# Optimization experiments

Hardware: AMD Instinct MI355X
Metric: run time of the kernel (lower is better)

## Reference

```python
import jax, jax.numpy as jnp
import numpy as np

SEQ, HID = 4096, 1024
NEG_INF = -10000000000.0


def setup_inputs() -> dict:
    key = jax.random.key(0)
    ks = jax.random.split(key, 6)
    s = 1.0 / np.sqrt(HID)
    return {
        "query": jax.random.normal(ks[0], (SEQ, HID), jnp.float32),
        "key": jax.random.normal(ks[1], (SEQ, HID), jnp.float32),
        "value": jax.random.normal(ks[2], (SEQ, HID), jnp.float32),
        # SASRec causal mask: allowed positions are 1, masked are 0
        "mask": jnp.tril(jnp.ones((SEQ, SEQ), jnp.int32)),
        "Wq": jax.random.normal(ks[3], (HID, HID), jnp.float32) * s,
        "Wk": jax.random.normal(ks[4], (HID, HID), jnp.float32) * s,
        "Wv": jax.random.normal(ks[5], (HID, HID), jnp.float32) * s,
    }


def reference(query, key, value, mask, Wq, Wk, Wv):
    # nn.Linear(bias=False): y = x @ W.T
    Q = query @ Wq.T   # [S, H]
    K = key @ Wk.T     # [S, H]
    V = value @ Wv.T   # [S, H]
    scale = jnp.sqrt(jnp.asarray(HID, Q.dtype))
    energy = (Q @ K.T) / scale                      # [S, S]
    energy = jnp.where(mask == 0, NEG_INF, energy)  # masked_fill
    attention = jax.nn.softmax(energy, axis=-1)     # [S, S]
    x = attention @ V                               # dropout is identity in eval
    return (x, attention)
```

## Files before the change

### kernel.cpp

```cpp
#include <hip/hip_runtime.h>

#define SEQ 4096
#define HID 1024

typedef _Float16 f16x4 __attribute__((ext_vector_type(4)));
typedef _Float16 f16x8 __attribute__((ext_vector_type(8)));
typedef float    f32x4 __attribute__((ext_vector_type(4)));

__device__ __forceinline__ void gld16(const void* g, void* l) {
    __builtin_amdgcn_global_load_lds(
        (const __attribute__((address_space(1))) unsigned int*)g,
        (__attribute__((address_space(3))) unsigned int*)l, 16, 0, 0);
}

__global__ __launch_bounds__(256) void cast_all(
    const float4* __restrict__ q, const float4* __restrict__ k,
    const float4* __restrict__ v,
    const float4* __restrict__ wq, const float4* __restrict__ wk,
    const float4* __restrict__ wv,
    f16x4* __restrict__ qh, f16x4* __restrict__ kh, f16x4* __restrict__ vh,
    f16x4* __restrict__ wqh, f16x4* __restrict__ wkh, f16x4* __restrict__ wvh,
    float4* __restrict__ zx,
    int nX4, int nW4, int nZ4) {
    int t = blockIdx.x * 256 + threadIdx.x;
    const float4 *a, *b, *c; f16x4 *da, *db, *dc; int idx;
    if (t < nX4) { a = q; b = k; c = v; da = qh; db = kh; dc = vh; idx = t; }
    else if (t < nX4 + nW4) {
        idx = t - nX4;
        a = wq; b = wk; c = wv; da = wqh; db = wkh; dc = wvh;
    } else {
        idx = t - nX4 - nW4;
        if (idx < nZ4) zx[idx] = float4{0.f, 0.f, 0.f, 0.f};
        return;
    }
    float4 va = a[idx], vb = b[idx], vc = c[idx];
    f16x4 oa = {(_Float16)va.x, (_Float16)va.y, (_Float16)va.z, (_Float16)va.w};
    f16x4 ob = {(_Float16)vb.x, (_Float16)vb.y, (_Float16)vb.z, (_Float16)vb.w};
    f16x4 oc = {(_Float16)vc.x, (_Float16)vc.y, (_Float16)vc.z, (_Float16)vc.w};
    da[idx] = oa; db[idx] = ob; dc[idx] = oc;
}

__global__ __launch_bounds__(256) void transpose_f16(
    const _Float16* __restrict__ src, _Float16* __restrict__ dst,
    int R, int C) {
    __shared__ _Float16 tile[32][33];
    int c0 = blockIdx.x * 32, r0 = blockIdx.y * 32;
    int tr = threadIdx.x >> 5, tc = threadIdx.x & 31;
#pragma unroll
    for (int q = 0; q < 4; ++q)
        tile[tr + q * 8][tc] = src[(size_t)(r0 + tr + q * 8) * C + c0 + tc];
    __syncthreads();
#pragma unroll
    for (int q = 0; q < 4; ++q)
        dst[(size_t)(c0 + tr + q * 8) * R + r0 + tc] = tile[tc][tr + q * 8];
}

template <typename OutT, bool TRI_SKIP, bool TRI_K, int ZMODE>
__global__ __launch_bounds__(256) void gemm_nt(
    const _Float16* __restrict__ A, const _Float16* __restrict__ Bt,
    OutT* __restrict__ C, int M, int N, int K, float scale,
    long sA, long sB, long sC, int KC) {
    __shared__ __attribute__((aligned(16))) _Float16 As[2 * 128 * 32];
    __shared__ __attribute__((aligned(16))) _Float16 Bs[2 * 128 * 32];

    int bm = blockIdx.y;
    const int bn = blockIdx.x;
    if (TRI_SKIP && bn > bm) return;
    if (ZMODE == 1) {
        A  += (long)blockIdx.z * sA;
        Bt += (long)blockIdx.z * sB;
        C  += (long)blockIdx.z * sC;
    }

    int kstart = 0, kend;
    bool single = false;
    if (ZMODE == 3) {
        int y = 143 - (int)blockIdx.y;
        int g = 0;
        while (2 * (g + 1) * (g + 2) <= y) ++g;
        const int rem = y - 2 * g * (g + 1);
        const int m   = g + 1;
        const int rg  = rem / m;
        bm = 4 * g + rg;
        const int zc = rem - rg * m;
        kstart = zc * KC;
        kend   = min((bm + 1) * 128, kstart + KC);
        single = (m == 1);
    } else {
        kend = TRI_K ? min(K, (bm + 1) * 128) : K;
        if (ZMODE == 2) {
            kstart = blockIdx.z * KC;
            if (kstart >= kend) return;
            single = (kend <= KC);
            kend = min(kend, kstart + KC);
        }
    }

    const int tid = threadIdx.x;
    const int tr  = tid >> 2;
    const int tc8 = (tid & 3) * 8;

    const _Float16* Ab = A  + (size_t)bm * 128 * K;
    const _Float16* Bb = Bt + (size_t)bn * 128 * K;

    const int wave = tid >> 6;
    const int lane = tid & 63;
    const int wm = (wave >> 1) * 64;
    const int wn = (wave & 1) * 64;
    const int lr = lane & 15;
    const int lk = (lane >> 4) * 8;

    f32x4 acc[4][4];
#pragma unroll
    for (int i = 0; i < 4; ++i)
#pragma unroll
        for (int j = 0; j < 4; ++j) acc[i][j] = (f32x4)0.0f;

    for (int k0 = kstart; k0 < kend; k0 += 64) {
#pragma unroll
        for (int h = 0; h < 2; ++h) {
            const int kk = k0 + h * 32, off = h * 4096;
            gld16(Ab + (size_t)tr * K        + kk + tc8, &As[off + tr * 32 + tc8]);
            gld16(Ab + (size_t)(64 + tr) * K + kk + tc8, &As[off + (64 + tr) * 32 + tc8]);
            gld16(Bb + (size_t)tr * K        + kk + tc8, &Bs[off + tr * 32 + tc8]);
            gld16(Bb + (size_t)(64 + tr) * K + kk + tc8, &Bs[off + (64 + tr) * 32 + tc8]);
        }
        __syncthreads();

#pragma unroll
        for (int h = 0; h < 2; ++h) {
            const int off = h * 4096;
            f16x8 af[4], bfr[4];
#pragma unroll
            for (int i = 0; i < 4; ++i)
                af[i] = *(const f16x8*)&As[off + (wm + i * 16 + lr) * 32 + lk];
#pragma unroll
            for (int j = 0; j < 4; ++j)
                bfr[j] = *(const f16x8*)&Bs[off + (wn + j * 16 + lr) * 32 + lk];
#pragma unroll
            for (int i = 0; i < 4; ++i)
#pragma unroll
                for (int j = 0; j < 4; ++j)
                    acc[i][j] = __builtin_amdgcn_mfma_f32_16x16x32_f16(
                        af[i], bfr[j], acc[i][j], 0, 0, 0);
        }
        __syncthreads();
    }

    const int er = (lane >> 4) * 4;
    const int ec = lane & 15;
#pragma unroll
    for (int i = 0; i < 4; ++i) {
#pragma unroll
        for (int j = 0; j < 4; ++j) {
            const int row0 = bm * 128 + wm + i * 16 + er;
            const int col  = bn * 128 + wn + j * 16 + ec;
#pragma unroll
            for (int r = 0; r < 4; ++r) {
                const size_t idx = (size_t)(row0 + r) * N + col;
                const float val = acc[i][j][r] * scale;
                if (ZMODE >= 2 && !single)
                    atomicAdd((float*)&C[idx], val);
                else
                    C[idx] = (OutT)val;
            }
        }
    }
}

__global__ __launch_bounds__(256) void softmax_causal(
    _Float16* __restrict__ EP, float* __restrict__ att, int S) {
    __shared__ float rowbuf[SEQ];
    __shared__ float red[8];
    const int i   = blockIdx.x;
    const int tid = threadIdx.x;
    const int wv  = tid >> 6, ln = tid & 63;
    _Float16* Erow = EP + (size_t)i * S;

    float lmax = -INFINITY;
    for (int j8 = tid * 8; j8 <= i; j8 += 2048) {
        f16x8 e8 = *(const f16x8*)&Erow[j8];
#pragma unroll
        for (int u = 0; u < 8; ++u) {
            int j = j8 + u;
            if (j <= i) {
                float vv = (float)e8[u];
                rowbuf[j] = vv;
                lmax = fmaxf(lmax, vv);
            }
        }
    }
#pragma unroll
    for (int o = 32; o > 0; o >>= 1) lmax = fmaxf(lmax, __shfl_down(lmax, o, 64));
    if (ln == 0) red[wv] = lmax;
    __syncthreads();
    if (tid == 0)
        red[4] = fmaxf(fmaxf(red[0], red[1]), fmaxf(red[2], red[3]));
    __syncthreads();
    const float rmax = red[4];

    float lsum = 0.0f;
    for (int j4 = tid * 4; j4 <= i; j4 += 1024) {
        float4 e = *(float4*)&rowbuf[j4];
        float4 o;
        o.x = (j4     <= i) ? __expf(e.x - rmax) : 0.f;
        o.y = (j4 + 1 <= i) ? __expf(e.y - rmax) : 0.f;
        o.z = (j4 + 2 <= i) ? __expf(e.z - rmax) : 0.f;
        o.w = (j4 + 3 <= i) ? __expf(e.w - rmax) : 0.f;
        *(float4*)&rowbuf[j4] = o;
        lsum += o.x + o.y + o.z + o.w;
    }
#pragma unroll
    for (int o = 32; o > 0; o >>= 1) lsum += __shfl_down(lsum, o, 64);
    __syncthreads();
    if (ln == 0) red[wv] = lsum;
    __syncthreads();
    if (tid == 0)
        red[4] = red[0] + red[1] + red[2] + red[3];
    __syncthreads();
    const float rinv = 1.0f / red[4];

    float* arow = att + (size_t)i * S;
    const int jlim = ((i >> 7) + 1) << 7;
    for (int j4 = tid * 4; j4 < S; j4 += 1024) {
        float4 a;
        a.x = (j4     <= i) ? rowbuf[j4]     * rinv : 0.f;
        a.y = (j4 + 1 <= i) ? rowbuf[j4 + 1] * rinv : 0.f;
        a.z = (j4 + 2 <= i) ? rowbuf[j4 + 2] * rinv : 0.f;
        a.w = (j4 + 3 <= i) ? rowbuf[j4 + 3] * rinv : 0.f;
        *(float4*)&arow[j4] = a;
        if (j4 < jlim) {
            f16x4 p = {(_Float16)a.x, (_Float16)a.y, (_Float16)a.z, (_Float16)a.w};
            *(f16x4*)&Erow[j4] = p;
        }
    }
}

extern "C" void kernel_launch(void* const* d_in, const int* in_sizes, int n_in,
                              void* d_out, int out_size, void* d_ws, size_t ws_size,
                              hipStream_t stream) {
    const float* q  = (const float*)d_in[0];
    const float* k  = (const float*)d_in[1];
    const float* v  = (const float*)d_in[2];
    const float* Wq = (const float*)d_in[4];
    const float* Wk = (const float*)d_in[5];
    const float* Wv = (const float*)d_in[6];

    float* out_x   = (float*)d_out;
    float* out_att = out_x + (size_t)SEQ * HID;

    char* ws = (char*)d_ws;
    const size_t SH = (size_t)SEQ * HID * sizeof(_Float16);
    const size_t HH = (size_t)HID * HID * sizeof(_Float16);
    _Float16* qh  = (_Float16*)(ws);
    _Float16* kh  = (_Float16*)(ws + SH);
    _Float16* vh  = (_Float16*)(ws + 2 * SH);
    _Float16* wqh = (_Float16*)(ws + 3 * SH);
    _Float16* wkh = (_Float16*)(ws + 3 * SH + HH);
    _Float16* wvh = (_Float16*)(ws + 3 * SH + 2 * HH);
    _Float16* Qh  = (_Float16*)(ws + 3 * SH + 3 * HH);
    _Float16* Kh  = (_Float16*)(ws + 4 * SH + 3 * HH);
    _Float16* Vh  = (_Float16*)(ws + 5 * SH + 3 * HH);
    _Float16* VT  = (_Float16*)(ws + 6 * SH + 3 * HH);
    _Float16* EP  = (_Float16*)(ws + 7 * SH + 3 * HH);

    const int nX4 = SEQ * HID / 4, nW4 = HID * HID / 4, nZ4 = SEQ * HID / 4;
    cast_all<<<(nX4 + nW4 + nZ4 + 255) / 256, 256, 0, stream>>>(
        (const float4*)q, (const float4*)k, (const float4*)v,
        (const float4*)Wq, (const float4*)Wk, (const float4*)Wv,
        (f16x4*)qh, (f16x4*)kh, (f16x4*)vh,
        (f16x4*)wqh, (f16x4*)wkh, (f16x4*)wvh,
        (float4*)out_x, nX4, nW4, nZ4);

    gemm_nt<_Float16, false, false, 1><<<dim3(HID / 128, SEQ / 128, 3), 256, 0, stream>>>(
        qh, wqh, Qh, SEQ, HID, HID, 1.0f,
        (long)SEQ * HID, (long)HID * HID, (long)SEQ * HID, 0);

    transpose_f16<<<dim3(HID / 32, SEQ / 32), 256, 0, stream>>>(Vh, VT, SEQ, HID);

    gemm_nt<_Float16, true, false, 0><<<dim3(SEQ / 128, SEQ / 128), 256, 0, stream>>>(
        Qh, Kh, EP, SEQ, SEQ, HID, 0.03125f, 0, 0, 0, 0);

    softmax_causal<<<SEQ, 256, 0, stream>>>(EP, out_att, SEQ);

    gemm_nt<float, false, true, 3><<<dim3(HID / 128, 144), 256, 0, stream>>>(
        EP, VT, out_x, SEQ, HID, SEQ, 1.0f, 0, 0, 0, 512);
}
```

Before: 344.3 us.

## Replace atomic split-K in PV GEMM with partial buffers and a reduce pass

```diff
diff --git a/kernel.cpp b/kernel.cpp
--- a/kernel.cpp
+++ b/kernel.cpp
@@ -20,19 +20,14 @@
     const float4* __restrict__ wv,
     f16x4* __restrict__ qh, f16x4* __restrict__ kh, f16x4* __restrict__ vh,
     f16x4* __restrict__ wqh, f16x4* __restrict__ wkh, f16x4* __restrict__ wvh,
-    float4* __restrict__ zx,
-    int nX4, int nW4, int nZ4) {
+    int nX4, int nW4) {
     int t = blockIdx.x * 256 + threadIdx.x;
     const float4 *a, *b, *c; f16x4 *da, *db, *dc; int idx;
     if (t < nX4) { a = q; b = k; c = v; da = qh; db = kh; dc = vh; idx = t; }
     else if (t < nX4 + nW4) {
         idx = t - nX4;
         a = wq; b = wk; c = wv; da = wqh; db = wkh; dc = wvh;
-    } else {
-        idx = t - nX4 - nW4;
-        if (idx < nZ4) zx[idx] = float4{0.f, 0.f, 0.f, 0.f};
-        return;
-    }
+    } else return;
     float4 va = a[idx], vb = b[idx], vc = c[idx];
     f16x4 oa = {(_Float16)va.x, (_Float16)va.y, (_Float16)va.z, (_Float16)va.w};
     f16x4 ob = {(_Float16)vb.x, (_Float16)vb.y, (_Float16)vb.z, (_Float16)vb.w};
@@ -59,7 +54,7 @@
 __global__ __launch_bounds__(256) void gemm_nt(
     const _Float16* __restrict__ A, const _Float16* __restrict__ Bt,
     OutT* __restrict__ C, int M, int N, int K, float scale,
-    long sA, long sB, long sC, int KC) {
+    long sA, long sB, long sC, int KC, float* __restrict__ PB) {
     __shared__ __attribute__((aligned(16))) _Float16 As[2 * 128 * 32];
     __shared__ __attribute__((aligned(16))) _Float16 Bs[2 * 128 * 32];
 
@@ -72,28 +67,21 @@
         C  += (long)blockIdx.z * sC;
     }
 
-    int kstart = 0, kend;
-    bool single = false;
-    if (ZMODE == 3) {
-        int y = 143 - (int)blockIdx.y;
+    int kstart = 0, kend, zslot = -1;
+    if (ZMODE == 4) {
+        const int y = 79 - (int)blockIdx.y;
         int g = 0;
-        while (2 * (g + 1) * (g + 2) <= y) ++g;
-        const int rem = y - 2 * g * (g + 1);
+        while (4 * (g + 1) * (g + 2) <= y) ++g;
+        const int rem = y - 4 * g * (g + 1);
         const int m   = g + 1;
         const int rg  = rem / m;
-        bm = 4 * g + rg;
-        const int zc = rem - rg * m;
-        kstart = zc * KC;
+        bm = 8 * g + rg;
+        const int z = rem - rg * m;
+        kstart = z * KC;
         kend   = min((bm + 1) * 128, kstart + KC);
-        single = (m == 1);
+        if (z > 0) zslot = 4 * g * (g - 1) + rg * g + (z - 1);
     } else {
         kend = TRI_K ? min(K, (bm + 1) * 128) : K;
-        if (ZMODE == 2) {
-            kstart = blockIdx.z * KC;
-            if (kstart >= kend) return;
-            single = (kend <= KC);
-            kend = min(kend, kstart + KC);
-        }
     }
 
     const int tid = threadIdx.x;
@@ -153,19 +141,35 @@
     for (int i = 0; i < 4; ++i) {
 #pragma unroll
         for (int j = 0; j < 4; ++j) {
-            const int row0 = bm * 128 + wm + i * 16 + er;
-            const int col  = bn * 128 + wn + j * 16 + ec;
+            const int lrow0 = wm + i * 16 + er;
+            const int col   = bn * 128 + wn + j * 16 + ec;
 #pragma unroll
             for (int r = 0; r < 4; ++r) {
-                const size_t idx = (size_t)(row0 + r) * N + col;
                 const float val = acc[i][j][r] * scale;
-                if (ZMODE >= 2 && !single)
-                    atomicAdd((float*)&C[idx], val);
+                if (ZMODE == 4 && zslot >= 0)
+                    PB[(size_t)(zslot * 128 + lrow0 + r) * 1024 + col] = val;
                 else
-                    C[idx] = (OutT)val;
+                    C[(size_t)(bm * 128 + lrow0 + r) * N + col] = (OutT)val;
             }
         }
     }
+}
+
+__global__ __launch_bounds__(256) void reduce_pv(
+    float* __restrict__ out, const float* __restrict__ PB) {
+    const int row = 1024 + blockIdx.x;
+    const int bm  = row >> 7;
+    const int g   = bm >> 3;
+    const int slot0 = 4 * g * (g - 1) + (bm - 8 * g) * g;
+    const int rloc  = row & 127;
+    float4* o = (float4*)(out + (size_t)row * 1024) + threadIdx.x;
+    float4 acc = *o;
+    for (int z = 0; z < g; ++z) {
+        const float4 p = *((const float4*)(PB +
+            ((size_t)(slot0 + z) * 128 + rloc) * 1024) + threadIdx.x);
+        acc.x += p.x; acc.y += p.y; acc.z += p.z; acc.w += p.w;
+    }
+    *o = acc;
 }
 
 __global__ __launch_bounds__(256) void softmax_causal(
@@ -263,26 +267,28 @@
     _Float16* Vh  = (_Float16*)(ws + 5 * SH + 3 * HH);
     _Float16* VT  = (_Float16*)(ws + 6 * SH + 3 * HH);
     _Float16* EP  = (_Float16*)(ws + 7 * SH + 3 * HH);
-
-    const int nX4 = SEQ * HID / 4, nW4 = HID * HID / 4, nZ4 = SEQ * HID / 4;
-    cast_all<<<(nX4 + nW4 + nZ4 + 255) / 256, 256, 0, stream>>>(
+    float* Pbuf = (float*)ws;
+
+    const int nX4 = SEQ * HID / 4, nW4 = HID * HID / 4;
+    cast_all<<<(nX4 + nW4 + 255) / 256, 256, 0, stream>>>(
         (const float4*)q, (const float4*)k, (const float4*)v,
         (const float4*)Wq, (const float4*)Wk, (const float4*)Wv,
         (f16x4*)qh, (f16x4*)kh, (f16x4*)vh,
-        (f16x4*)wqh, (f16x4*)wkh, (f16x4*)wvh,
-        (float4*)out_x, nX4, nW4, nZ4);
+        (f16x4*)wqh, (f16x4*)wkh, (f16x4*)wvh, nX4, nW4);
 
     gemm_nt<_Float16, false, false, 1><<<dim3(HID / 128, SEQ / 128, 3), 256, 0, stream>>>(
         qh, wqh, Qh, SEQ, HID, HID, 1.0f,
-        (long)SEQ * HID, (long)HID * HID, (long)SEQ * HID, 0);
+        (long)SEQ * HID, (long)HID * HID, (long)SEQ * HID, 0, nullptr);
 
     transpose_f16<<<dim3(HID / 32, SEQ / 32), 256, 0, stream>>>(Vh, VT, SEQ, HID);
 
     gemm_nt<_Float16, true, false, 0><<<dim3(SEQ / 128, SEQ / 128), 256, 0, stream>>>(
-        Qh, Kh, EP, SEQ, SEQ, HID, 0.03125f, 0, 0, 0, 0);
+        Qh, Kh, EP, SEQ, SEQ, HID, 0.03125f, 0, 0, 0, 0, nullptr);
 
     softmax_causal<<<SEQ, 256, 0, stream>>>(EP, out_att, SEQ);
 
-    gemm_nt<float, false, true, 3><<<dim3(HID / 128, 144), 256, 0, stream>>>(
-        EP, VT, out_x, SEQ, HID, SEQ, 1.0f, 0, 0, 0, 512);
-}
+    gemm_nt<float, false, true, 4><<<dim3(HID / 128, 80), 256, 0, stream>>>(
+        EP, VT, out_x, SEQ, HID, SEQ, 1.0f, 0, 0, 0, 1024, Pbuf);
+
+    reduce_pv<<<3072, 256, 0, stream>>>(out_x, Pbuf);
+}
```

Measured after the change: 315.7 us. -8.3%, faster.
